# Kernel optimization log

Hardware: AMD Instinct MI355X
Metric: run time of the kernel (lower is better)

Reference implementation:

```python
import jax, jax.numpy as jnp
import numpy as np

B, C, H, W = 8, 64, 496, 432
P = 96000  # total non-empty pillars across the batch


def setup_inputs() -> dict:
    key = jax.random.key(0)
    k1, k2, k3, k4 = jax.random.split(key, 4)
    voxel_features = jax.random.normal(k1, (P, C), dtype=jnp.float32)
    b = jax.random.randint(k2, (P,), 0, B)
    y = jax.random.randint(k3, (P,), 0, H)
    x = jax.random.randint(k4, (P,), 0, W)
    z = jnp.zeros((P,), dtype=jnp.int32)
    coords = jnp.stack([b.astype(jnp.int32), z, y.astype(jnp.int32), x.astype(jnp.int32)], axis=1)  # [P,4] = (batch, z, y, x)
    return {"voxel_features": voxel_features, "coords": coords, "batch_size": B}


def reference(voxel_features, coords, batch_size):
    # Flattened scatter: canvas[b, :, y, x] = voxel_features[p, :]
    flat_idx = coords[:, 0].astype(jnp.int32) * (H * W) + coords[:, 2].astype(jnp.int32) * W + coords[:, 3].astype(jnp.int32)  # [P]
    canvas = jnp.zeros((batch_size * H * W, C), dtype=voxel_features.dtype)
    canvas = canvas.at[flat_idx].set(voxel_features)
    return canvas.reshape(batch_size, H, W, C).transpose(0, 3, 1, 2)  # [B, C, H, W]
```

## Files before the change

### kernel.cpp

```cpp
#include <hip/hip_runtime.h>


constexpr int HH  = 496;
constexpr int WW  = 432;
constexpr int CC  = 64;
constexpr int HWp = HH * WW;
constexpr int W4  = WW / 4;
constexpr int QPB   = 32;
constexpr int CELLS = QPB * 4;
constexpr int PAD   = 65;

typedef float v4f __attribute__((ext_vector_type(4)));

__device__ float g_zero_row[CC];

__global__ void k_winner(const int* __restrict__ coords, int* __restrict__ winner,
                         int wstride, int P) {
    int p = blockIdx.x * blockDim.x + threadIdx.x;
    if (p >= P) return;
    int4 c4 = reinterpret_cast<const int4*>(coords)[p];
    atomicMax(&winner[c4.x * wstride + c4.z * WW + c4.w], p + 1);
}

__global__ __launch_bounds__(256) void k_gather_lds(
        const float* __restrict__ feat, const int* __restrict__ winner,
        float* __restrict__ out, int blocksPerBatch) {
    __shared__ float rows[CELLS * PAD];

    const int bb       = blockIdx.x / blocksPerBatch;
    const int cellbase = (blockIdx.x % blocksPerBatch) * (QPB * 4);
    const int t   = threadIdx.x;
    const int grp = t >> 4;
    const int ln  = t & 15;

    const int* wbase = winner + bb * HWp + cellbase;

    #pragma unroll
    for (int r = 0; r < 8; ++r) {
        int row = r * 16 + grp;
        int w = wbase[row];
        v4f v = {0.0f, 0.0f, 0.0f, 0.0f};
        if (w > 0)
            v = *reinterpret_cast<const v4f*>(feat + (size_t)(w - 1) * CC + ln * 4);
        *reinterpret_cast<v4f*>(&rows[row * PAD + ln * 4]) = v;
    }
    __syncthreads();

    const int qv = t & 31;
    const int cg = t >> 5;
    float* obase = out + (size_t)bb * CC * HWp + cellbase;
    #pragma unroll
    for (int r = 0; r < 8; ++r) {
        int c = r * 8 + cg;
        v4f s;
        s.x = rows[(qv * 4 + 0) * PAD + c];
        s.y = rows[(qv * 4 + 1) * PAD + c];
        s.z = rows[(qv * 4 + 2) * PAD + c];
        s.w = rows[(qv * 4 + 3) * PAD + c];
        __builtin_nontemporal_store(
            s, reinterpret_cast<v4f*>(obase + (size_t)c * HWp + qv * 4));
    }
}

__global__ __launch_bounds__(256) void k_gather_cells(
        const float* __restrict__ feat, const int* __restrict__ winner,
        int wstride, float* __restrict__ out, int total) {
    int t = blockIdx.x * blockDim.x + threadIdx.x;
    if (t >= total) return;
    int x4 = t % W4;  int r = t / W4;
    int y  = r % HH;  int bb = r / HH;
    const int4 win = *reinterpret_cast<const int4*>(
        &winner[bb * wstride + y * WW + x4 * 4]);
    const float* f0 = (win.x > 0) ? feat + (size_t)(win.x - 1) * CC : g_zero_row;
    const float* f1 = (win.y > 0) ? feat + (size_t)(win.y - 1) * CC : g_zero_row;
    const float* f2 = (win.z > 0) ? feat + (size_t)(win.z - 1) * CC : g_zero_row;
    const float* f3 = (win.w > 0) ? feat + (size_t)(win.w - 1) * CC : g_zero_row;
    float* ob = out + ((size_t)bb * CC * HH + y) * WW + x4 * 4;
    #pragma unroll 4
    for (int cq = 0; cq < CC / 4; ++cq) {
        v4f a = *reinterpret_cast<const v4f*>(f0 + cq * 4);
        v4f b = *reinterpret_cast<const v4f*>(f1 + cq * 4);
        v4f c = *reinterpret_cast<const v4f*>(f2 + cq * 4);
        v4f d = *reinterpret_cast<const v4f*>(f3 + cq * 4);
        float* o = ob + (size_t)cq * 4 * HWp;
        v4f s0 = {a.x, b.x, c.x, d.x};
        v4f s1 = {a.y, b.y, c.y, d.y};
        v4f s2 = {a.z, b.z, c.z, d.z};
        v4f s3 = {a.w, b.w, c.w, d.w};
        __builtin_nontemporal_store(s0, reinterpret_cast<v4f*>(o));
        __builtin_nontemporal_store(s1, reinterpret_cast<v4f*>(o + HWp));
        __builtin_nontemporal_store(s2, reinterpret_cast<v4f*>(o + 2 * HWp));
        __builtin_nontemporal_store(s3, reinterpret_cast<v4f*>(o + 3 * HWp));
    }
}

extern "C" void kernel_launch(void* const* d_in, const int* in_sizes, int n_in,
                              void* d_out, int out_size, void* d_ws, size_t ws_size,
                              hipStream_t stream) {
    const float* feat   = (const float*)d_in[0];
    const int*   coords = (const int*)d_in[1];
    float*       out    = (float*)d_out;

    const int P = in_sizes[0] / CC;
    const int B = out_size / (CC * HWp);

    const size_t winner_bytes = (size_t)B * HWp * sizeof(int);

    if (ws_size >= winner_bytes) {
        int* winner = (int*)d_ws;
        hipMemsetAsync(winner, 0, winner_bytes, stream);
        k_winner<<<(P + 255) / 256, 256, 0, stream>>>(coords, winner, HWp, P);
        const int blocksPerBatch = (HH * W4) / QPB;
        const int nblocks = B * blocksPerBatch;
        k_gather_lds<<<nblocks, 256, 0, stream>>>(feat, winner, out, blocksPerBatch);
    } else {
        for (int b = 0; b < B; ++b)
            hipMemsetAsync(out + (size_t)b * CC * HWp, 0,
                           (size_t)HWp * sizeof(int), stream);
        k_winner<<<(P + 255) / 256, 256, 0, stream>>>(
            coords, (int*)out, CC * HWp, P);
        const int total = B * HH * W4;
        k_gather_cells<<<(total + 255) / 256, 256, 0, stream>>>(
            feat, (int*)out, CC * HWp, out, total);
    }
}
```

Before: 94.85 us.

## Add channel-group pipelined gather kernel with 1024-cell blocks

Adds a new gather kernel in which each 256-thread block owns 1024 consecutive flattened cells. It loops over 16 channel groups: it loads a 4-channel slice of each cell's winner row, transposes it through LDS, and writes coalesced rows for 4 channels. Blocks may straddle a batch boundary, so the output batch index is computed per store. This cuts LDS footprint and raises occupancy, and lengthens the contiguous output runs per channel. The cost is 32 barriers per block and feature rows read in 16-byte pieces across iterations instead of all at once.

```diff
diff --git a/kernel.cpp b/kernel.cpp
--- a/kernel.cpp
+++ b/kernel.cpp
@@ -6,9 +6,11 @@
 constexpr int CC  = 64;
 constexpr int HWp = HH * WW;
 constexpr int W4  = WW / 4;
+constexpr int CELLS = 1024;
+constexpr int PADR  = 1028;
 constexpr int QPB   = 32;
-constexpr int CELLS = QPB * 4;
-constexpr int PAD   = 65;
+constexpr int CELLS6 = 128;
+constexpr int PAD6   = 65;
 
 typedef float v4f __attribute__((ext_vector_type(4)));
 
@@ -22,10 +24,59 @@
     atomicMax(&winner[c4.x * wstride + c4.z * WW + c4.w], p + 1);
 }
 
+__global__ __launch_bounds__(256) void k_gather_pipe(
+        const float* __restrict__ feat, const int* __restrict__ winner,
+        float* __restrict__ out) {
+    __shared__ float stg[4 * PADR];
+
+    const int g0    = blockIdx.x * CELLS;
+    const int bb    = g0 / HWp;
+    const int bound = (bb + 1) * HWp;
+    const int t   = threadIdx.x;
+    const int wid = t >> 6;
+    const int qv  = t & 63;
+
+    int wreg[4];
+    const float* fp[4];
+    #pragma unroll
+    for (int k = 0; k < 4; ++k) {
+        wreg[k] = winner[g0 + t + 256 * k];
+        fp[k] = feat + (size_t)(wreg[k] - 1) * CC;
+    }
+
+    for (int grp = 0; grp < 16; ++grp) {
+        #pragma unroll
+        for (int k = 0; k < 4; ++k) {
+            int cell = t + 256 * k;
+            v4f v = {0.0f, 0.0f, 0.0f, 0.0f};
+            if (wreg[k] > 0)
+                v = *reinterpret_cast<const v4f*>(fp[k] + grp * 4);
+            stg[0 * PADR + cell] = v.x;
+            stg[1 * PADR + cell] = v.y;
+            stg[2 * PADR + cell] = v.z;
+            stg[3 * PADR + cell] = v.w;
+        }
+        __syncthreads();
+
+        const int c = grp * 4 + wid;
+        #pragma unroll
+        for (int k = 0; k < 4; ++k) {
+            int cell = (k * 64 + qv) * 4;
+            int g = g0 + cell;
+            int b = (g >= bound) ? bb + 1 : bb;
+            int i = g - b * HWp;
+            v4f s = *reinterpret_cast<const v4f*>(&stg[wid * PADR + cell]);
+            __builtin_nontemporal_store(
+                s, reinterpret_cast<v4f*>(out + ((size_t)b * CC + c) * HWp + i));
+        }
+        __syncthreads();
+    }
+}
+
 __global__ __launch_bounds__(256) void k_gather_lds(
         const float* __restrict__ feat, const int* __restrict__ winner,
         float* __restrict__ out, int blocksPerBatch) {
-    __shared__ float rows[CELLS * PAD];
+    __shared__ float rows[CELLS6 * PAD6];
 
     const int bb       = blockIdx.x / blocksPerBatch;
     const int cellbase = (blockIdx.x % blocksPerBatch) * (QPB * 4);
@@ -42,7 +93,7 @@
         v4f v = {0.0f, 0.0f, 0.0f, 0.0f};
         if (w > 0)
             v = *reinterpret_cast<const v4f*>(feat + (size_t)(w - 1) * CC + ln * 4);
-        *reinterpret_cast<v4f*>(&rows[row * PAD + ln * 4]) = v;
+        *reinterpret_cast<v4f*>(&rows[row * PAD6 + ln * 4]) = v;
     }
     __syncthreads();
 
@@ -53,10 +104,10 @@
     for (int r = 0; r < 8; ++r) {
         int c = r * 8 + cg;
         v4f s;
-        s.x = rows[(qv * 4 + 0) * PAD + c];
-        s.y = rows[(qv * 4 + 1) * PAD + c];
-        s.z = rows[(qv * 4 + 2) * PAD + c];
-        s.w = rows[(qv * 4 + 3) * PAD + c];
+        s.x = rows[(qv * 4 + 0) * PAD6 + c];
+        s.y = rows[(qv * 4 + 1) * PAD6 + c];
+        s.z = rows[(qv * 4 + 2) * PAD6 + c];
+        s.w = rows[(qv * 4 + 3) * PAD6 + c];
         __builtin_nontemporal_store(
             s, reinterpret_cast<v4f*>(obase + (size_t)c * HWp + qv * 4));
     }
@@ -103,16 +154,22 @@
 
     const int P = in_sizes[0] / CC;
     const int B = out_size / (CC * HWp);
+    const int totalCells = B * HWp;
 
-    const size_t winner_bytes = (size_t)B * HWp * sizeof(int);
+    const size_t winner_bytes = (size_t)totalCells * sizeof(int);
 
     if (ws_size >= winner_bytes) {
         int* winner = (int*)d_ws;
         hipMemsetAsync(winner, 0, winner_bytes, stream);
         k_winner<<<(P + 255) / 256, 256, 0, stream>>>(coords, winner, HWp, P);
-        const int blocksPerBatch = (HH * W4) / QPB;
-        const int nblocks = B * blocksPerBatch;
-        k_gather_lds<<<nblocks, 256, 0, stream>>>(feat, winner, out, blocksPerBatch);
+        if (totalCells % CELLS == 0) {
+            k_gather_pipe<<<totalCells / CELLS, 256, 0, stream>>>(
+                feat, winner, out);
+        } else {
+            const int blocksPerBatch = (HH * W4) / QPB;
+            k_gather_lds<<<B * blocksPerBatch, 256, 0, stream>>>(
+                feat, winner, out, blocksPerBatch);
+        }
     } else {
         for (int b = 0; b < B; ++b)
             hipMemsetAsync(out + (size_t)b * CC * HWp, 0,
```

After: 98.66 us. 1.04x slower.
